# Kernel optimization log

Measured on AMD Instinct MI355X. Metric: run time of the kernel, lower is better.

## Reference

```python
import jax, jax.numpy as jnp
import numpy as np

# Static module config (must match init_kwargs / input_specs)
C, HEADS, POINTS, LEVELS = 256, 8, 8, 2
H, W = 128, 128           # BEV grid per agent/level
NQ = H * W                # num_query = H*W
DH = C // HEADS           # per-head dim


def setup_inputs() -> dict:
    key = jax.random.key(0)
    ks = jax.random.split(key, 12)
    s = 0.02
    return {
        "query": jax.random.normal(ks[0], (1, NQ, C), jnp.float32),
        "query_pos": jax.random.normal(ks[1], (1, NQ, C), jnp.float32),
        "value": jax.random.normal(ks[2], (LEVELS, NQ, C), jnp.float32),
        "reference_points": jax.random.uniform(ks[3], (1, NQ, LEVELS, 2), jnp.float32),
        "spatial_shapes": jnp.full((LEVELS, 2), H, dtype=jnp.int32),
        "W_off": jax.random.normal(ks[4], (C, LEVELS * HEADS * POINTS * 2), jnp.float32) * s,
        "b_off": jax.random.normal(ks[5], (LEVELS * HEADS * POINTS * 2,), jnp.float32) * s,
        "W_attn": jax.random.normal(ks[6], (C, LEVELS * HEADS * POINTS), jnp.float32) * s,
        "b_attn": jax.random.normal(ks[7], (LEVELS * HEADS * POINTS,), jnp.float32) * s,
        "W_val": jax.random.normal(ks[8], (C, C), jnp.float32) * s,
        "b_val": jax.random.normal(ks[9], (C,), jnp.float32) * s,
        "W_out": jax.random.normal(ks[10], (C, C), jnp.float32) * s,
        "b_out": jax.random.normal(ks[11], (C,), jnp.float32) * s,
    }


def _bilinear(img, x, y):
    """grid_sample-style bilinear, align_corners=False, zero padding.
    img: (H, W, D); x, y: (...) pixel-space coords. Returns (..., D)."""
    Hh, Ww = img.shape[0], img.shape[1]
    x0f, y0f = jnp.floor(x), jnp.floor(y)
    x0, y0 = x0f.astype(jnp.int32), y0f.astype(jnp.int32)
    x1, y1 = x0 + 1, y0 + 1
    wx1, wy1 = x - x0f, y - y0f
    wx0, wy0 = 1.0 - wx1, 1.0 - wy1

    def gather(yy, xx):
        valid = (yy >= 0) & (yy < Hh) & (xx >= 0) & (xx < Ww)
        g = img[jnp.clip(yy, 0, Hh - 1), jnp.clip(xx, 0, Ww - 1)]
        return jnp.where(valid[..., None], g, 0.0)

    return (gather(y0, x0) * (wy0 * wx0)[..., None]
            + gather(y0, x1) * (wy0 * wx1)[..., None]
            + gather(y1, x0) * (wy1 * wx0)[..., None]
            + gather(y1, x1) * (wy1 * wx1)[..., None])


_sample_heads = jax.vmap(_bilinear, in_axes=(0, 0, 0))  # over heads


def reference(query, query_pos, value, reference_points, spatial_shapes,
              W_off, b_off, W_attn, b_attn, W_val, b_val, W_out, b_out):
    identity = query                                        # (1, NQ, C)
    q = (query + query_pos)[0]                              # (NQ, C), bs=1

    v = value @ W_val + b_val                               # (L, NQ, C)
    v = v.reshape(LEVELS, H, W, HEADS, DH)                  # per-level feature maps

    off = (q @ W_off + b_off).reshape(NQ, HEADS, LEVELS, POINTS, 2)
    attn = (q @ W_attn + b_attn).reshape(NQ, HEADS, LEVELS * POINTS)
    attn = jax.nn.softmax(attn, axis=-1).reshape(NQ, HEADS, LEVELS, POINTS)

    # offset_normalizer = (W, H) per level
    norm = jnp.stack([spatial_shapes[:, 1], spatial_shapes[:, 0]], -1).astype(q.dtype)  # (L, 2)
    # sampling_locations in normalized [0,1] coords: (NQ, HEADS, LEVELS, POINTS, 2)
    loc = reference_points[0][:, None, :, None, :] + off / norm[None, None, :, None, :]

    out = jnp.zeros((NQ, HEADS, DH), dtype=q.dtype)
    for l in range(LEVELS):
        img_l = jnp.transpose(v[l], (2, 0, 1, 3))           # (HEADS, H, W, DH)
        # align_corners=False: px = x_norm * W - 0.5
        xl = jnp.transpose(loc[:, :, l, :, 0], (1, 0, 2)) * W - 0.5  # (HEADS, NQ, POINTS)
        yl = jnp.transpose(loc[:, :, l, :, 1], (1, 0, 2)) * H - 0.5
        sampled = _sample_heads(img_l, xl, yl)              # (HEADS, NQ, POINTS, DH)
        out = out + jnp.einsum('hqpd,qhp->qhd', sampled, attn[:, :, l, :])

    out = out.reshape(NQ, C) @ W_out + b_out                # (NQ, C)
    return out[None] + identity                             # dropout is identity (eval / p=0)
```

## Files before the change

### kernel.cpp

```cpp
#include <hip/hip_runtime.h>
#include <hip/hip_bf16.h>
#include <math.h>

#define NQ     16384
#define CDIM   256
#define NHEADS 8
#define NPTS   8
#define NLVL   2
#define HH     128
#define WWID   128
#define DHEAD  32
#define NCAT   384

#define PW        130
#define CELLB     32
#define ROWB      (PW * CELLB)
#define MAPB      (PW * PW * CELLB)
#define V2BYTES   (NLVL * NHEADS * MAPB)
#define MEMSET_BLKS 2113
#define TRANS_BLKS  224
#define CONVV_BLKS  4096
#define CONVQ_BLKS  2048

typedef __bf16 bf16_t;
typedef __bf16 bf16x8 __attribute__((ext_vector_type(8)));
typedef float  f32x4  __attribute__((ext_vector_type(4)));
typedef float  f32x2  __attribute__((ext_vector_type(2)));

typedef __attribute__((address_space(1))) const uint32_t gau32;
typedef __attribute__((address_space(3))) uint32_t lau32;

__device__ __forceinline__ bf16_t f2b(float f) { return (bf16_t)f; }

__device__ __forceinline__ bf16x8 cvt8(float4 a, float4 b) {
    bf16x8 v;
    v[0] = f2b(a.x); v[1] = f2b(a.y); v[2] = f2b(a.z); v[3] = f2b(a.w);
    v[4] = f2b(b.x); v[5] = f2b(b.y); v[6] = f2b(b.z); v[7] = f2b(b.w);
    return v;
}

__global__ __launch_bounds__(256) void prep_k(const float* __restrict__ W_val,
                                              const float* __restrict__ W_off,
                                              const float* __restrict__ W_attn,
                                              const float* __restrict__ W_out,
                                              const float* __restrict__ value,
                                              const float* __restrict__ query,
                                              const float* __restrict__ query_pos,
                                              unsigned char* __restrict__ v2,
                                              bf16_t* __restrict__ Wt_val,
                                              bf16_t* __restrict__ Wt_qa,
                                              bf16_t* __restrict__ Wt_out,
                                              bf16_t* __restrict__ value_bf16,
                                              bf16_t* __restrict__ qsum) {
    const int b = blockIdx.x;
    if (b < MEMSET_BLKS) {
        size_t off = ((size_t)b * 256 + threadIdx.x) * 16;
        if (off < V2BYTES)
            *reinterpret_cast<uint4*>(v2 + off) = make_uint4(0, 0, 0, 0);
        return;
    }
    if (b < MEMSET_BLKS + TRANS_BLKS) {
        const int tb = b - MEMSET_BLKS;
        const float* W; bf16_t* Wt; int N, t; bool permute = false;
        if (tb < 64)       { W = W_val;  Wt = Wt_val;            N = 256; t = tb;       permute = true; }
        else if (tb < 128) { W = W_off;  Wt = Wt_qa;             N = 256; t = tb - 64;  }
        else if (tb < 160) { W = W_attn; Wt = Wt_qa + 256 * 256; N = 128; t = tb - 128; }
        else               { W = W_out;  Wt = Wt_out;            N = 256; t = tb - 160; }
        const int ntn = N >> 5;
        const int k0 = (t / ntn) * 32, n0 = (t % ntn) * 32;
        const int tx = threadIdx.x & 31, ty = threadIdx.x >> 5;
        __shared__ float s[32][33];
#pragma unroll
        for (int i = 0; i < 4; ++i)
            s[ty + 8 * i][tx] = W[(size_t)(k0 + ty + 8 * i) * N + n0 + tx];
        __syncthreads();
#pragma unroll
        for (int i = 0; i < 4; ++i) {
            const int n = n0 + ty + 8 * i;
            const int p = permute ? ((n & ~63) | ((n & 3) << 4) | ((n & 63) >> 2)) : n;
            Wt[(size_t)p * 256 + k0 + tx] = f2b(s[tx][ty + 8 * i]);
        }
        return;
    }
    if (b < MEMSET_BLKS + TRANS_BLKS + CONVV_BLKS) {
        const size_t off = ((size_t)(b - MEMSET_BLKS - TRANS_BLKS) * 256 + threadIdx.x) * 8;
        float4 a = *reinterpret_cast<const float4*>(value + off);
        float4 c = *reinterpret_cast<const float4*>(value + off + 4);
        *reinterpret_cast<bf16x8*>(value_bf16 + off) = cvt8(a, c);
        return;
    }
    {
        const size_t off =
            ((size_t)(b - MEMSET_BLKS - TRANS_BLKS - CONVV_BLKS) * 256 + threadIdx.x) * 8;
        float4 a0 = *reinterpret_cast<const float4*>(query + off);
        float4 a1 = *reinterpret_cast<const float4*>(query + off + 4);
        float4 b0 = *reinterpret_cast<const float4*>(query_pos + off);
        float4 b1 = *reinterpret_cast<const float4*>(query_pos + off + 4);
        a0.x += b0.x; a0.y += b0.y; a0.z += b0.z; a0.w += b0.w;
        a1.x += b1.x; a1.y += b1.y; a1.z += b1.z; a1.w += b1.w;
        *reinterpret_cast<bf16x8*>(qsum + off) = cvt8(a0, a1);
    }
}

template <bool OUT_BF16, bool ADD_SRC, bool PERM_V>
__device__ __forceinline__ void gemm_body(bf16_t (&As)[128][64], bf16_t (&Bs)[128][64],
                                          int bidx, int bidy,
                                          const bf16_t* __restrict__ Abf,
                                          const bf16_t* __restrict__ Bt,
                                          const float* __restrict__ bias,
                                          const float* __restrict__ bias2,
                                          int Nsplit,
                                          const float* __restrict__ addsrc,
                                          void* __restrict__ Cout,
                                          int N, int K) {
    const int tid  = threadIdx.x;
    const int wave = tid >> 6;
    const int lane = tid & 63;
    const int rowBase = bidy * 128;
    const int colBase = bidx * 128;
    const int wm = (wave & 1) * 64;
    const int wn = (wave >> 1) * 64;
    const int fr = lane & 15;
    const int fq = lane >> 4;

    f32x4 acc[4][4] = {};

    const int lrow = lane >> 3;
    const int scol = ((lane & 7) ^ lrow) * 8;

    for (int k0 = 0; k0 < K; k0 += 64) {
        __syncthreads();
#pragma unroll
        for (int t = 0; t < 4; ++t) {
            const bf16_t* src =
                Abf + (size_t)(rowBase + wave * 32 + t * 8 + lrow) * K + k0 + scol;
            __builtin_amdgcn_global_load_lds((gau32*)src,
                                             (lau32*)&As[wave * 32 + t * 8][0],
                                             16, 0, 0);
        }
#pragma unroll
        for (int t = 0; t < 4; ++t) {
            const bf16_t* src =
                Bt + (size_t)(colBase + wave * 32 + t * 8 + lrow) * K + k0 + scol;
            __builtin_amdgcn_global_load_lds((gau32*)src,
                                             (lau32*)&Bs[wave * 32 + t * 8][0],
                                             16, 0, 0);
        }
        __syncthreads();
#pragma unroll
        for (int ks = 0; ks < 2; ++ks) {
            const int gk = ((ks * 4 + fq) ^ (fr & 7)) * 8;
            bf16x8 af[4], bfr[4];
#pragma unroll
            for (int i = 0; i < 4; ++i)
                af[i] = *reinterpret_cast<const bf16x8*>(&As[wm + i * 16 + fr][gk]);
#pragma unroll
            for (int j = 0; j < 4; ++j)
                bfr[j] = *reinterpret_cast<const bf16x8*>(&Bs[wn + j * 16 + fr][gk]);
#pragma unroll
            for (int i = 0; i < 4; ++i)
#pragma unroll
                for (int j = 0; j < 4; ++j)
                    acc[i][j] = __builtin_amdgcn_mfma_f32_16x16x32_bf16(af[i], bfr[j],
                                                                        acc[i][j], 0, 0, 0);
        }
    }

    if (PERM_V) {
        const int lbase = colBase + wn + fr * 4;
        const float bv0 = bias[lbase], bv1 = bias[lbase + 1];
        const float bv2 = bias[lbase + 2], bv3 = bias[lbase + 3];
        const int hh = (lbase >> 5) & 7;
        const int dbase = lbase & 31;
        unsigned char* outp = (unsigned char*)Cout;
#pragma unroll
        for (int i = 0; i < 4; ++i) {
#pragma unroll
            for (int r = 0; r < 4; ++r) {
                const int row = rowBase + wm + i * 16 + fq * 4 + r;
                const int lv = row >> 14, cell = row & 16383;
                const int y = cell >> 7, x = cell & 127;
                uint32_t pk = __builtin_amdgcn_cvt_pk_fp8_f32(
                    acc[i][0][r] + bv0, acc[i][1][r] + bv1, 0, false);
                pk = (uint32_t)__builtin_amdgcn_cvt_pk_fp8_f32(
                    acc[i][2][r] + bv2, acc[i][3][r] + bv3, pk, true);
                *reinterpret_cast<uint32_t*>(
                    outp + (size_t)(lv * NHEADS + hh) * MAPB
                         + (size_t)(y + 1) * ROWB + (x + 1) * CELLB + dbase) = pk;
            }
        }
        return;
    }

#pragma unroll
    for (int j = 0; j < 4; ++j) {
        const int col = colBase + wn + j * 16 + fr;
        const float bv = (col < Nsplit) ? bias[col] : bias2[col - Nsplit];
#pragma unroll
        for (int i = 0; i < 4; ++i) {
#pragma unroll
            for (int r = 0; r < 4; ++r) {
                const int row = rowBase + wm + i * 16 + fq * 4 + r;
                float vv = acc[i][j][r] + bv;
                if (ADD_SRC) vv += addsrc[(size_t)row * N + col];
                if (OUT_BF16)
                    ((bf16_t*)Cout)[(size_t)row * N + col] = f2b(vv);
                else
                    ((float*)Cout)[(size_t)row * N + col] = vv;
            }
        }
    }
}

__global__ __launch_bounds__(256, 4) void fused_proj_k(const bf16_t* __restrict__ value_bf16,
                                                       const bf16_t* __restrict__ qsum,
                                                       const bf16_t* __restrict__ Wt_val,
                                                       const bf16_t* __restrict__ Wt_qa,
                                                       const float* __restrict__ b_val,
                                                       const float* __restrict__ b_off,
                                                       const float* __restrict__ b_attn,
                                                       unsigned char* __restrict__ v2,
                                                       bf16_t* __restrict__ cbuf) {
    __shared__ __align__(16) bf16_t As[128][64];
    __shared__ __align__(16) bf16_t Bs[128][64];
    const int b = blockIdx.x;
    if (b < 512) {
        const int bidy = (b >> 4) * 8 + (b & 7);
        const int bidx = (b >> 3) & 1;
        gemm_body<true, false, true>(As, Bs, bidx, bidy, value_bf16,
                                     Wt_val, b_val, b_val, 256, nullptr, v2,
                                     CDIM, CDIM);
    } else {
        const int b2 = b - 512;
        const int bidy = (b2 / 24) * 8 + (b2 & 7);
        const int bidx = (b2 >> 3) % 3;
        gemm_body<true, false, false>(As, Bs, bidx, bidy, qsum,
                                      Wt_qa, b_off, b_attn, 256, nullptr, cbuf,
                                      NCAT, CDIM);
    }
}

__global__ __launch_bounds__(256, 3) void outproj_k(const bf16_t* __restrict__ tmp,
                                                    const bf16_t* __restrict__ Wt_out,
                                                    const float* __restrict__ b_out,
                                                    const float* __restrict__ query,
                                                    float* __restrict__ out) {
    __shared__ __align__(16) bf16_t As[128][64];
    __shared__ __align__(16) bf16_t Bs[128][64];
    const int b = blockIdx.x;
    const int bidy = (b >> 4) * 8 + (b & 7);
    const int bidx = (b >> 3) & 1;
    gemm_body<false, true, false>(As, Bs, bidx, bidy, tmp,
                                  Wt_out, b_out, b_out, 256, query, out,
                                  CDIM, CDIM);
}

__device__ __forceinline__ void acc_tap4(uint4 u, float w, f32x2* acc2) {
    acc2[0] += __builtin_amdgcn_cvt_pk_f32_fp8((int)u.x, false) * w;
    acc2[1] += __builtin_amdgcn_cvt_pk_f32_fp8((int)u.x, true)  * w;
    acc2[2] += __builtin_amdgcn_cvt_pk_f32_fp8((int)u.y, false) * w;
    acc2[3] += __builtin_amdgcn_cvt_pk_f32_fp8((int)u.y, true)  * w;
    acc2[4] += __builtin_amdgcn_cvt_pk_f32_fp8((int)u.z, false) * w;
    acc2[5] += __builtin_amdgcn_cvt_pk_f32_fp8((int)u.z, true)  * w;
    acc2[6] += __builtin_amdgcn_cvt_pk_f32_fp8((int)u.w, false) * w;
    acc2[7] += __builtin_amdgcn_cvt_pk_f32_fp8((int)u.w, true)  * w;
}

__global__ __launch_bounds__(256) void sample_k(const unsigned char* __restrict__ v2,
                                                const bf16_t* __restrict__ cbuf,
                                                const float* __restrict__ refp,
                                                bf16_t* __restrict__ tmp) {
    const int b    = blockIdx.x;
    const int h    = b & 7;
    const int qblk = b >> 3;
    const int tid  = threadIdx.x;
    const int qloc = tid >> 1;
    const int ck   = tid & 1;
    const int q    = qblk * 128 + qloc;

    const bf16_t* qrow = cbuf + (size_t)q * NCAT;
    const float4 rp = *reinterpret_cast<const float4*>(refp + (size_t)q * 4);

    const bf16_t* attp = qrow + 256 + h * 16;
    bf16x8 A0 = *reinterpret_cast<const bf16x8*>(attp);
    bf16x8 A1 = *reinterpret_cast<const bf16x8*>(attp + 8);
    float e[16];
#pragma unroll
    for (int i = 0; i < 8; ++i) { e[i] = (float)A0[i]; e[8 + i] = (float)A1[i]; }
    float m = e[0];
#pragma unroll
    for (int i = 1; i < 16; ++i) m = fmaxf(m, e[i]);
    float s = 0.f;
#pragma unroll
    for (int i = 0; i < 16; ++i) { e[i] = __expf(e[i] - m); s += e[i]; }
    const float inv = 1.f / s;
#pragma unroll
    for (int i = 0; i < 16; ++i) e[i] *= inv;

    f32x2 acc2[8] = {};

#pragma unroll
    for (int l = 0; l < NLVL; ++l) {
        const float bx = (l == 0 ? rp.x : rp.z) * (float)WWID - 0.5f;
        const float by = (l == 0 ? rp.y : rp.w) * (float)HH - 0.5f;
        const unsigned char* base = v2 + (size_t)(l * NHEADS + h) * MAPB
                                       + 131 * CELLB + ck * 16;
        const bf16_t* offp = qrow + h * 32 + l * 16;
        bf16x8 o0 = *reinterpret_cast<const bf16x8*>(offp);
        bf16x8 o1 = *reinterpret_cast<const bf16x8*>(offp + 8);
        float ox[8], oy[8];
#pragma unroll
        for (int i = 0; i < 4; ++i) {
            ox[i]     = (float)o0[2 * i];  oy[i]     = (float)o0[2 * i + 1];
            ox[4 + i] = (float)o1[2 * i];  oy[4 + i] = (float)o1[2 * i + 1];
        }

#pragma unroll
        for (int p = 0; p < NPTS; ++p) {
            const float px = bx + ox[p];
            const float py = by + oy[p];
            const float w  = e[l * 8 + p];
            const float x0f = floorf(px), y0f = floorf(py);
            const int x0 = (int)x0f, y0 = (int)y0f;
            const float wx1 = px - x0f, wy1 = py - y0f;
            const float wx0 = 1.f - wx1, wy0 = 1.f - wy1;
            const int x0c = min(max(x0, -1), 128);
            const int x1c = min(max(x0 + 1, -1), 128);
            const int y0c = min(max(y0, -1), 128);
            const int y1c = min(max(y0 + 1, -1), 128);
            const unsigned char* r0 = base + y0c * ROWB;
            const unsigned char* r1 = base + y1c * ROWB;
            uint4 u00 = *reinterpret_cast<const uint4*>(r0 + x0c * CELLB);
            uint4 u10 = *reinterpret_cast<const uint4*>(r0 + x1c * CELLB);
            uint4 u01 = *reinterpret_cast<const uint4*>(r1 + x0c * CELLB);
            uint4 u11 = *reinterpret_cast<const uint4*>(r1 + x1c * CELLB);
            const float wy0w = w * wy0, wy1w = w * wy1;
            acc_tap4(u00, wy0w * wx0, acc2);
            acc_tap4(u10, wy0w * wx1, acc2);
            acc_tap4(u01, wy1w * wx0, acc2);
            acc_tap4(u11, wy1w * wx1, acc2);
        }
    }

    bf16x8 ov0, ov1;
#pragma unroll
    for (int i = 0; i < 4; ++i) {
        ov0[2 * i]     = f2b(acc2[i].x);
        ov0[2 * i + 1] = f2b(acc2[i].y);
        ov1[2 * i]     = f2b(acc2[4 + i].x);
        ov1[2 * i + 1] = f2b(acc2[4 + i].y);
    }
    bf16_t* op = tmp + (size_t)q * CDIM + h * DHEAD + ck * 16;
    *reinterpret_cast<bf16x8*>(op)     = ov0;
    *reinterpret_cast<bf16x8*>(op + 8) = ov1;
}

extern "C" void kernel_launch(void* const* d_in, const int* in_sizes, int n_in,
                              void* d_out, int out_size, void* d_ws, size_t ws_size,
                              hipStream_t stream) {
    const float* query     = (const float*)d_in[0];
    const float* query_pos = (const float*)d_in[1];
    const float* value     = (const float*)d_in[2];
    const float* refp      = (const float*)d_in[3];
    const float* W_off  = (const float*)d_in[5];
    const float* b_off  = (const float*)d_in[6];
    const float* W_attn = (const float*)d_in[7];
    const float* b_attn = (const float*)d_in[8];
    const float* W_val  = (const float*)d_in[9];
    const float* b_val  = (const float*)d_in[10];
    const float* W_out  = (const float*)d_in[11];
    const float* b_out  = (const float*)d_in[12];
    float* out = (float*)d_out;

    char* ws = (char*)d_ws;
    unsigned char* v2 = (unsigned char*)(ws);
    bf16_t* cbuf    = (bf16_t*)(ws + 8654848);
    bf16_t* tmp     = (bf16_t*)(ws + 21237760);
    bf16_t* Wt_val  = (bf16_t*)(ws + 29626368);
    bf16_t* Wt_qa   = (bf16_t*)(ws + 29757440);
    bf16_t* Wt_out  = (bf16_t*)(ws + 29954048);
    bf16_t* qsum       = tmp;
    bf16_t* value_bf16 = (bf16_t*)d_out;

    prep_k<<<MEMSET_BLKS + TRANS_BLKS + CONVV_BLKS + CONVQ_BLKS, 256, 0, stream>>>(
        W_val, W_off, W_attn, W_out, value, query, query_pos,
        v2, Wt_val, Wt_qa, Wt_out, value_bf16, qsum);
    fused_proj_k<<<896, 256, 0, stream>>>(value_bf16, qsum,
                                          Wt_val, Wt_qa, b_val, b_off, b_attn,
                                          v2, cbuf);
    sample_k<<<1024, 256, 0, stream>>>(v2, cbuf, refp, tmp);
    outproj_k<<<256, 256, 0, stream>>>(tmp, Wt_out, b_out, query, out);
}
```

Before: 192.7 us.

## Fuse fp32-to-bf16 conversion and query add into projection GEMM loads; zero only borders

The fp32 value and query+query_pos inputs are now read directly inside the projection GEMM, which adds them, converts to bf16 and stores the tiles into LDS. This removes the separate conversion pass and its bf16 intermediate round trip through global memory. The full memset of the padded value map is replaced by zeroing only the one-cell border, assuming the GEMM writes every interior cell. In exchange the GEMM loads fp32 through registers instead of direct global-to-LDS loads, raising register pressure, so the launch bound drops from 4 to 3 blocks.

```diff
diff --git a/kernel.cpp b/kernel.cpp
--- a/kernel.cpp
+++ b/kernel.cpp
@@ -16,11 +16,8 @@
 #define CELLB     32
 #define ROWB      (PW * CELLB)
 #define MAPB      (PW * PW * CELLB)
-#define V2BYTES   (NLVL * NHEADS * MAPB)
-#define MEMSET_BLKS 2113
+#define BORDER_BLKS 16
 #define TRANS_BLKS  224
-#define CONVV_BLKS  4096
-#define CONVQ_BLKS  2048
 
 typedef __bf16 bf16_t;
 typedef __bf16 bf16x8 __attribute__((ext_vector_type(8)));
@@ -43,24 +40,27 @@
                                               const float* __restrict__ W_off,
                                               const float* __restrict__ W_attn,
                                               const float* __restrict__ W_out,
-                                              const float* __restrict__ value,
-                                              const float* __restrict__ query,
-                                              const float* __restrict__ query_pos,
                                               unsigned char* __restrict__ v2,
                                               bf16_t* __restrict__ Wt_val,
                                               bf16_t* __restrict__ Wt_qa,
-                                              bf16_t* __restrict__ Wt_out,
-                                              bf16_t* __restrict__ value_bf16,
-                                              bf16_t* __restrict__ qsum) {
+                                              bf16_t* __restrict__ Wt_out) {
     const int b = blockIdx.x;
-    if (b < MEMSET_BLKS) {
-        size_t off = ((size_t)b * 256 + threadIdx.x) * 16;
-        if (off < V2BYTES)
-            *reinterpret_cast<uint4*>(v2 + off) = make_uint4(0, 0, 0, 0);
+    if (b < BORDER_BLKS) {
+        unsigned char* map = v2 + (size_t)b * MAPB;
+        for (int i = threadIdx.x; i < 516; i += 256) {
+            int y, x;
+            if (i < 130)      { y = 0;        x = i;       }
+            else if (i < 260) { y = 129;      x = i - 130; }
+            else if (i < 388) { y = i - 259;  x = 0;       }
+            else              { y = i - 387;  x = 129;     }
+            uint4* p = reinterpret_cast<uint4*>(map + (size_t)y * ROWB + x * CELLB);
+            p[0] = make_uint4(0, 0, 0, 0);
+            p[1] = make_uint4(0, 0, 0, 0);
+        }
         return;
     }
-    if (b < MEMSET_BLKS + TRANS_BLKS) {
-        const int tb = b - MEMSET_BLKS;
+    {
+        const int tb = b - BORDER_BLKS;
         const float* W; bf16_t* Wt; int N, t; bool permute = false;
         if (tb < 64)       { W = W_val;  Wt = Wt_val;            N = 256; t = tb;       permute = true; }
         else if (tb < 128) { W = W_off;  Wt = Wt_qa;             N = 256; t = tb - 64;  }
@@ -80,32 +80,15 @@
             const int p = permute ? ((n & ~63) | ((n & 3) << 4) | ((n & 63) >> 2)) : n;
             Wt[(size_t)p * 256 + k0 + tx] = f2b(s[tx][ty + 8 * i]);
         }
-        return;
-    }
-    if (b < MEMSET_BLKS + TRANS_BLKS + CONVV_BLKS) {
-        const size_t off = ((size_t)(b - MEMSET_BLKS - TRANS_BLKS) * 256 + threadIdx.x) * 8;
-        float4 a = *reinterpret_cast<const float4*>(value + off);
-        float4 c = *reinterpret_cast<const float4*>(value + off + 4);
-        *reinterpret_cast<bf16x8*>(value_bf16 + off) = cvt8(a, c);
-        return;
-    }
-    {
-        const size_t off =
-            ((size_t)(b - MEMSET_BLKS - TRANS_BLKS - CONVV_BLKS) * 256 + threadIdx.x) * 8;
-        float4 a0 = *reinterpret_cast<const float4*>(query + off);
-        float4 a1 = *reinterpret_cast<const float4*>(query + off + 4);
-        float4 b0 = *reinterpret_cast<const float4*>(query_pos + off);
-        float4 b1 = *reinterpret_cast<const float4*>(query_pos + off + 4);
-        a0.x += b0.x; a0.y += b0.y; a0.z += b0.z; a0.w += b0.w;
-        a1.x += b1.x; a1.y += b1.y; a1.z += b1.z; a1.w += b1.w;
-        *reinterpret_cast<bf16x8*>(qsum + off) = cvt8(a0, a1);
-    }
-}
-
-template <bool OUT_BF16, bool ADD_SRC, bool PERM_V>
+    }
+}
+
+template <int AMODE, bool OUT_BF16, bool ADD_SRC, bool PERM_V>
 __device__ __forceinline__ void gemm_body(bf16_t (&As)[128][64], bf16_t (&Bs)[128][64],
                                           int bidx, int bidy,
                                           const bf16_t* __restrict__ Abf,
+                                          const float* __restrict__ Af0,
+                                          const float* __restrict__ Af1,
                                           const bf16_t* __restrict__ Bt,
                                           const float* __restrict__ bias,
                                           const float* __restrict__ bias2,
@@ -130,13 +113,33 @@
 
     for (int k0 = 0; k0 < K; k0 += 64) {
         __syncthreads();
-#pragma unroll
-        for (int t = 0; t < 4; ++t) {
-            const bf16_t* src =
-                Abf + (size_t)(rowBase + wave * 32 + t * 8 + lrow) * K + k0 + scol;
-            __builtin_amdgcn_global_load_lds((gau32*)src,
-                                             (lau32*)&As[wave * 32 + t * 8][0],
-                                             16, 0, 0);
+        float4 ra[4][2], rb[4][2];
+        if constexpr (AMODE == 0) {
+#pragma unroll
+            for (int t = 0; t < 4; ++t) {
+                const bf16_t* src =
+                    Abf + (size_t)(rowBase + wave * 32 + t * 8 + lrow) * K + k0 + scol;
+                __builtin_amdgcn_global_load_lds((gau32*)src,
+                                                 (lau32*)&As[wave * 32 + t * 8][0],
+                                                 16, 0, 0);
+            }
+        } else {
+#pragma unroll
+            for (int t = 0; t < 4; ++t) {
+                const float* src =
+                    Af0 + (size_t)(rowBase + wave * 32 + t * 8 + lrow) * K + k0 + scol;
+                ra[t][0] = *reinterpret_cast<const float4*>(src);
+                ra[t][1] = *reinterpret_cast<const float4*>(src + 4);
+            }
+            if constexpr (AMODE == 2) {
+#pragma unroll
+                for (int t = 0; t < 4; ++t) {
+                    const float* src =
+                        Af1 + (size_t)(rowBase + wave * 32 + t * 8 + lrow) * K + k0 + scol;
+                    rb[t][0] = *reinterpret_cast<const float4*>(src);
+                    rb[t][1] = *reinterpret_cast<const float4*>(src + 4);
+                }
+            }
         }
 #pragma unroll
         for (int t = 0; t < 4; ++t) {
@@ -145,6 +148,20 @@
             __builtin_amdgcn_global_load_lds((gau32*)src,
                                              (lau32*)&Bs[wave * 32 + t * 8][0],
                                              16, 0, 0);
+        }
+        if constexpr (AMODE != 0) {
+#pragma unroll
+            for (int t = 0; t < 4; ++t) {
+                float4 a = ra[t][0], c = ra[t][1];
+                if constexpr (AMODE == 2) {
+                    a.x += rb[t][0].x; a.y += rb[t][0].y;
+                    a.z += rb[t][0].z; a.w += rb[t][0].w;
+                    c.x += rb[t][1].x; c.y += rb[t][1].y;
+                    c.z += rb[t][1].z; c.w += rb[t][1].w;
+                }
+                *reinterpret_cast<bf16x8*>(
+                    &As[wave * 32 + t * 8 + lrow][(lane & 7) * 8]) = cvt8(a, c);
+            }
         }
         __syncthreads();
 #pragma unroll
@@ -212,8 +229,9 @@
     }
 }
 
-__global__ __launch_bounds__(256, 4) void fused_proj_k(const bf16_t* __restrict__ value_bf16,
-                                                       const bf16_t* __restrict__ qsum,
+__global__ __launch_bounds__(256, 3) void fused_proj_k(const float* __restrict__ value,
+                                                       const float* __restrict__ query,
+                                                       const float* __restrict__ query_pos,
                                                        const bf16_t* __restrict__ Wt_val,
                                                        const bf16_t* __restrict__ Wt_qa,
                                                        const float* __restrict__ b_val,
@@ -227,16 +245,16 @@
     if (b < 512) {
         const int bidy = (b >> 4) * 8 + (b & 7);
         const int bidx = (b >> 3) & 1;
-        gemm_body<true, false, true>(As, Bs, bidx, bidy, value_bf16,
-                                     Wt_val, b_val, b_val, 256, nullptr, v2,
-                                     CDIM, CDIM);
+        gemm_body<1, true, false, true>(As, Bs, bidx, bidy, nullptr, value, nullptr,
+                                        Wt_val, b_val, b_val, 256, nullptr, v2,
+                                        CDIM, CDIM);
     } else {
         const int b2 = b - 512;
         const int bidy = (b2 / 24) * 8 + (b2 & 7);
         const int bidx = (b2 >> 3) % 3;
-        gemm_body<true, false, false>(As, Bs, bidx, bidy, qsum,
-                                      Wt_qa, b_off, b_attn, 256, nullptr, cbuf,
-                                      NCAT, CDIM);
+        gemm_body<2, true, false, false>(As, Bs, bidx, bidy, nullptr, query, query_pos,
+                                         Wt_qa, b_off, b_attn, 256, nullptr, cbuf,
+                                         NCAT, CDIM);
     }
 }
 
@@ -250,9 +268,9 @@
     const int b = blockIdx.x;
     const int bidy = (b >> 4) * 8 + (b & 7);
     const int bidx = (b >> 3) & 1;
-    gemm_body<false, true, false>(As, Bs, bidx, bidy, tmp,
-                                  Wt_out, b_out, b_out, 256, query, out,
-                                  CDIM, CDIM);
+    gemm_body<0, false, true, false>(As, Bs, bidx, bidy, tmp, nullptr, nullptr,
+                                     Wt_out, b_out, b_out, 256, query, out,
+                                     CDIM, CDIM);
 }
 
 __device__ __forceinline__ void acc_tap4(uint4 u, float w, f32x2* acc2) {
@@ -379,13 +397,10 @@
     bf16_t* Wt_val  = (bf16_t*)(ws + 29626368);
     bf16_t* Wt_qa   = (bf16_t*)(ws + 29757440);
     bf16_t* Wt_out  = (bf16_t*)(ws + 29954048);
-    bf16_t* qsum       = tmp;
-    bf16_t* value_bf16 = (bf16_t*)d_out;
-
-    prep_k<<<MEMSET_BLKS + TRANS_BLKS + CONVV_BLKS + CONVQ_BLKS, 256, 0, stream>>>(
-        W_val, W_off, W_attn, W_out, value, query, query_pos,
-        v2, Wt_val, Wt_qa, Wt_out, value_bf16, qsum);
-    fused_proj_k<<<896, 256, 0, stream>>>(value_bf16, qsum,
+
+    prep_k<<<BORDER_BLKS + TRANS_BLKS, 256, 0, stream>>>(
+        W_val, W_off, W_attn, W_out, v2, Wt_val, Wt_qa, Wt_out);
+    fused_proj_k<<<896, 256, 0, stream>>>(value, query, query_pos,
                                           Wt_val, Wt_qa, b_val, b_off, b_attn,
                                           v2, cbuf);
     sample_k<<<1024, 256, 0, stream>>>(v2, cbuf, refp, tmp);
```

After: 181.5 us. 1.06x faster.
